# Kernel tuning notes

Measured on AMD Instinct MI355X. Metric: run time of the kernel, lower is better.

Reference implementation:

```python
import jax, jax.numpy as jnp
import numpy as np

NBITS = 4
GROUP = 128
K = 4096   # in_features
N = 4096   # out_features
M = 4096   # flattened batch*seq tokens
EPS = 32 // NBITS  # elements per packed int32 = 8
MASK = (1 << NBITS) - 1  # unpack_mask = 15


def setup_inputs() -> dict:
    key = jax.random.key(0)
    k1, k2, k3, k4, k5 = jax.random.split(key, 5)
    x = jax.random.normal(k1, (M, K), dtype=jnp.float32)
    # raw 4-bit quantized weights, layout [K, N] (i.e. W_q.t() from the torch module)
    nib = jax.random.randint(k2, (K, N), 0, 1 << NBITS, dtype=jnp.int32)
    # pack EPS nibbles per int32 along K, matching pack(): element j gets shift j*NBITS
    nib = nib.reshape(K // EPS, EPS, N)
    shifts = (jnp.arange(EPS, dtype=jnp.int32) * NBITS)[None, :, None]
    parts = nib << shifts  # disjoint bit ranges
    W_q_packed = parts[:, 0]
    for j in range(1, EPS):
        W_q_packed = W_q_packed | parts[:, j]
    W_q_packed = W_q_packed.astype(jnp.int32)  # [K//EPS, N]
    # group-wise scales/zeros: [K//GROUP, N] (scales.view(N,-1).t() layout)
    scales = (jax.random.uniform(k3, (K // GROUP, N), dtype=jnp.float32) + 0.5) * 0.01
    zeros = jax.random.uniform(k4, (K // GROUP, N), dtype=jnp.float32) * MASK
    bias = jax.random.normal(k5, (N,), dtype=jnp.float32) * 0.1
    return {"x": x, "W_q_packed": W_q_packed, "scales": scales, "zeros": zeros, "bias": bias}


def reference(x, W_q_packed, scales, zeros, bias):
    # unpack: w[k, n] = (packed[k//EPS, n] >> ((k % EPS) * NBITS)) & MASK
    shifts = (jnp.arange(EPS, dtype=jnp.int32) * NBITS)[None, :, None]
    w = (W_q_packed[:, None, :] >> shifts) & MASK  # [K//EPS, EPS, N]
    w = w.reshape(K, N).astype(jnp.float32)
    # group-wise asymmetric dequant (W_group_mode == 3): W = (w - z) * s
    s = jnp.repeat(scales, GROUP, axis=0)  # [K, N]
    z = jnp.repeat(zeros, GROUP, axis=0)   # [K, N]
    W = (w - z) * s
    out = x @ W + bias  # [M, N]
    return out
```

## Files before the change

### kernel.cpp

```cpp
#include <hip/hip_runtime.h>
#include <stdint.h>


#define M_DIM 4096
#define N_DIM 4096
#define K_DIM 4096

typedef __attribute__((ext_vector_type(8))) short short8;
typedef __attribute__((ext_vector_type(4))) float f32x4;

__device__ __forceinline__ unsigned short f2bf(float f) {
  uint32_t u = __builtin_bit_cast(uint32_t, f);
  u += 0x7fffu + ((u >> 16) & 1u);
  return (unsigned short)(u >> 16);
}

__global__ __launch_bounds__(256) void cvt_kernel(const float* __restrict__ x,
                                                  unsigned short* __restrict__ xb) {
  const int tid = threadIdx.x;
  const int total = (M_DIM * K_DIM) / 8;
  const float4* x4 = (const float4*)x;
  uint4* o8 = (uint4*)xb;
#pragma unroll
  for (int p = 0; p < 4; ++p) {
    int i = (p * 2048 + blockIdx.x) * 256 + tid;
    if (i < total) {
      float4 a = x4[2 * i], b = x4[2 * i + 1];
      uint4 o;
      o.x = (uint32_t)f2bf(a.x) | ((uint32_t)f2bf(a.y) << 16);
      o.y = (uint32_t)f2bf(a.z) | ((uint32_t)f2bf(a.w) << 16);
      o.z = (uint32_t)f2bf(b.x) | ((uint32_t)f2bf(b.y) << 16);
      o.w = (uint32_t)f2bf(b.z) | ((uint32_t)f2bf(b.w) << 16);
      o8[i] = o;
    }
  }
}

__global__ __launch_bounds__(256) void dequant_kernel(const int* __restrict__ Wq,
                                                      const float* __restrict__ scales,
                                                      const float* __restrict__ zeros,
                                                      unsigned short* __restrict__ wt) {
  __shared__ uint4 Ts[32 * 64];
  const int tid = threadIdx.x;
  const int blk = blockIdx.x;
  const int n0 = (blk & 127) * 32;
  const int gk0 = (blk >> 7) * 64;

#pragma unroll
  for (int p = 0; p < 8; ++p) {
    int e = p * 256 + tid;
    int n_l = e & 31;
    int gk_l = e >> 5;
    int gk = gk0 + gk_l;
    int n = n0 + n_l;
    int g = gk >> 4;
    uint32_t q = (uint32_t)Wq[gk * N_DIM + n];
    float s = scales[g * N_DIM + n];
    float z = zeros[g * N_DIM + n];
    unsigned short b[8];
#pragma unroll
    for (int j = 0; j < 8; ++j) {
      float f = ((float)((q >> (4 * j)) & 15u) - z) * s;
      b[j] = f2bf(f);
    }
    uint4 cell;
    cell.x = (uint32_t)b[0] | ((uint32_t)b[1] << 16);
    cell.y = (uint32_t)b[2] | ((uint32_t)b[3] << 16);
    cell.z = (uint32_t)b[4] | ((uint32_t)b[5] << 16);
    cell.w = (uint32_t)b[6] | ((uint32_t)b[7] << 16);
    Ts[n_l * 64 + (gk_l ^ (n_l & 7))] = cell;
  }
  __syncthreads();
  uint4* dst = (uint4*)wt;
#pragma unroll
  for (int p = 0; p < 8; ++p) {
    int n_l = p * 4 + (tid >> 6);
    int gk_l = tid & 63;
    uint4 cell = Ts[n_l * 64 + (gk_l ^ (n_l & 7))];
    dst[(size_t)(n0 + n_l) * (K_DIM / 8) + (gk0 + gk_l)] = cell;
  }
}


#define ASBUF(T) (As + ((T) & 1) * 1024)
#define BSBUF(T) (Bs + ((T) & 1) * 512)

#define GLDS(DST, SRC)                                                          \
  __builtin_amdgcn_global_load_lds(                                             \
      (const __attribute__((address_space(1))) void*)(SRC),                     \
      (__attribute__((address_space(3))) void*)(DST), 16, 0, 0)

#define STAGE(T)                                                                \
  {                                                                             \
    const unsigned short* as = Asrc + (size_t)(T) * 32;                         \
    const unsigned short* bs = Bsrc + (size_t)(T) * 32;                         \
    GLDS(ASBUF(T) + tid, as);                                                   \
    GLDS(ASBUF(T) + tid + 512, as + (size_t)128 * K_DIM);                       \
    GLDS(BSBUF(T) + tid, bs);                                                   \
  }

#define SB0 __builtin_amdgcn_sched_barrier(0)

__global__ __launch_bounds__(512, 4) void gemm_bt_kernel(
    const unsigned short* __restrict__ A, const unsigned short* __restrict__ Bt,
    const float* __restrict__ bias, float* __restrict__ C) {
  __shared__ short8 As[2 * 1024];
  __shared__ short8 Bs[2 * 512];

  const int tid = threadIdx.x;
  const int lane = tid & 63;
  const int w = tid >> 6;
  const int wm = w >> 1;
  const int wn = w & 1;

  const int b = blockIdx.x;
  const int xcd = b & 7;
  const int loc = b >> 3;
  const int nt = xcd * 4 + (loc & 3);
  const int mt = loc >> 2;
  const int m0 = mt * 256;
  const int n0 = nt * 128;

  const int srow = tid >> 2;
  const int skc = (tid & 3) ^ ((srow >> 1) & 3);
  const unsigned short* Asrc = A + (size_t)(m0 + srow) * K_DIM + skc * 8;
  const unsigned short* Bsrc = Bt + (size_t)(n0 + srow) * K_DIM + skc * 8;

  const int fr = lane & 15;
  const int fc = lane >> 4;
  const int kxs = fc ^ ((fr >> 1) & 3);
  const int a_b = (wm * 64 + fr) * 4 + kxs;
  const int b_b = (wn * 64 + fr) * 4 + kxs;

  f32x4 acc[4][4] = {};

  STAGE(0);
  asm volatile("s_waitcnt vmcnt(0)" ::: "memory");
  SB0;
  __builtin_amdgcn_s_barrier();

  for (int t = 0; t < 128; ++t) {
    if (t < 127) STAGE(t + 1);

    const short8* ASb = ASBUF(t);
    const short8* BSb = BSBUF(t);
    short8 af[4], bv[4];
#pragma unroll
    for (int mi = 0; mi < 4; ++mi) af[mi] = ASb[a_b + mi * 64];
#pragma unroll
    for (int ni = 0; ni < 4; ++ni) bv[ni] = BSb[b_b + ni * 64];

    __builtin_amdgcn_s_setprio(1);
#pragma unroll
    for (int mi = 0; mi < 4; ++mi)
#pragma unroll
      for (int ni = 0; ni < 4; ++ni)
        acc[mi][ni] = __builtin_amdgcn_mfma_f32_16x16x32_bf16(af[mi], bv[ni],
                                                              acc[mi][ni], 0, 0, 0);
    __builtin_amdgcn_s_setprio(0);

    if (t < 127) {
      asm volatile("s_waitcnt vmcnt(0)" ::: "memory");
      SB0;
      __builtin_amdgcn_s_barrier();
      SB0;
    }
  }

  const int rr = (lane >> 4) * 4;
#pragma unroll
  for (int ni = 0; ni < 4; ++ni) {
    const int gn = n0 + wn * 64 + ni * 16 + fr;
    const float bvv = bias[gn];
#pragma unroll
    for (int mi = 0; mi < 4; ++mi) {
      const int gm = m0 + wm * 64 + mi * 16 + rr;
#pragma unroll
      for (int r = 0; r < 4; ++r)
        C[(size_t)(gm + r) * N_DIM + gn] = acc[mi][ni][r] + bvv;
    }
  }
}

extern "C" void kernel_launch(void* const* d_in, const int* in_sizes, int n_in,
                              void* d_out, int out_size, void* d_ws, size_t ws_size,
                              hipStream_t stream) {
  const float* x = (const float*)d_in[0];
  const int* wq = (const int*)d_in[1];
  const float* sc = (const float*)d_in[2];
  const float* zr = (const float*)d_in[3];
  const float* bias = (const float*)d_in[4];
  float* out = (float*)d_out;

  unsigned short* xb = (unsigned short*)d_ws;
  unsigned short* wt = (unsigned short*)((char*)d_ws + (size_t)M_DIM * K_DIM * 2);

  cvt_kernel<<<dim3(2048), dim3(256), 0, stream>>>(x, xb);
  dequant_kernel<<<dim3(1024), dim3(256), 0, stream>>>(wq, sc, zr, wt);
  gemm_bt_kernel<<<dim3(512), dim3(512), 0, stream>>>(xb, wt, bias, out);
}
```

Measured before the change: 269.4 us.

## Pre-swizzle dequantized weights into MFMA fragment layout and load B directly to registers

```diff
diff --git a/kernel.cpp b/kernel.cpp
--- a/kernel.cpp
+++ b/kernel.cpp
@@ -39,133 +39,136 @@
 __global__ __launch_bounds__(256) void dequant_kernel(const int* __restrict__ Wq,
                                                       const float* __restrict__ scales,
                                                       const float* __restrict__ zeros,
-                                                      unsigned short* __restrict__ wt) {
-  __shared__ uint4 Ts[32 * 64];
+                                                      uint4* __restrict__ wf) {
   const int tid = threadIdx.x;
-  const int blk = blockIdx.x;
-  const int n0 = (blk & 127) * 32;
-  const int gk0 = (blk >> 7) * 64;
-
-#pragma unroll
-  for (int p = 0; p < 8; ++p) {
-    int e = p * 256 + tid;
-    int n_l = e & 31;
-    int gk_l = e >> 5;
-    int gk = gk0 + gk_l;
-    int n = n0 + n_l;
+#pragma unroll
+  for (int p = 0; p < 4; ++p) {
+    int c = (p * 2048 + blockIdx.x) * 256 + tid;
+    int lane = c & 63;
+    int F = c >> 6;
+    int t = F & 127;
+    int nf = F >> 7;
+    int fr = lane & 15, fc = lane >> 4;
+    int n = nf * 16 + fr;
+    int gk = t * 4 + fc;
     int g = gk >> 4;
     uint32_t q = (uint32_t)Wq[gk * N_DIM + n];
     float s = scales[g * N_DIM + n];
     float z = zeros[g * N_DIM + n];
-    unsigned short b[8];
+    unsigned short bb[8];
 #pragma unroll
     for (int j = 0; j < 8; ++j) {
       float f = ((float)((q >> (4 * j)) & 15u) - z) * s;
-      b[j] = f2bf(f);
+      bb[j] = f2bf(f);
     }
     uint4 cell;
-    cell.x = (uint32_t)b[0] | ((uint32_t)b[1] << 16);
-    cell.y = (uint32_t)b[2] | ((uint32_t)b[3] << 16);
-    cell.z = (uint32_t)b[4] | ((uint32_t)b[5] << 16);
-    cell.w = (uint32_t)b[6] | ((uint32_t)b[7] << 16);
-    Ts[n_l * 64 + (gk_l ^ (n_l & 7))] = cell;
-  }
-  __syncthreads();
-  uint4* dst = (uint4*)wt;
-#pragma unroll
-  for (int p = 0; p < 8; ++p) {
-    int n_l = p * 4 + (tid >> 6);
-    int gk_l = tid & 63;
-    uint4 cell = Ts[n_l * 64 + (gk_l ^ (n_l & 7))];
-    dst[(size_t)(n0 + n_l) * (K_DIM / 8) + (gk0 + gk_l)] = cell;
-  }
-}
-
-
-#define ASBUF(T) (As + ((T) & 1) * 1024)
-#define BSBUF(T) (Bs + ((T) & 1) * 512)
+    cell.x = (uint32_t)bb[0] | ((uint32_t)bb[1] << 16);
+    cell.y = (uint32_t)bb[2] | ((uint32_t)bb[3] << 16);
+    cell.z = (uint32_t)bb[4] | ((uint32_t)bb[5] << 16);
+    cell.w = (uint32_t)bb[6] | ((uint32_t)bb[7] << 16);
+    wf[c] = cell;
+  }
+}
+
 
 #define GLDS(DST, SRC)                                                          \
   __builtin_amdgcn_global_load_lds(                                             \
       (const __attribute__((address_space(1))) void*)(SRC),                     \
       (__attribute__((address_space(3))) void*)(DST), 16, 0, 0)
 
-#define STAGE(T)                                                                \
+#define SB0 __builtin_amdgcn_sched_barrier(0)
+#define VM2 asm volatile("s_waitcnt vmcnt(2)" ::: "memory")
+#define VM0 asm volatile("s_waitcnt vmcnt(0)" ::: "memory")
+
+#define LOADB(DST, T)                                                           \
   {                                                                             \
-    const unsigned short* as = Asrc + (size_t)(T) * 32;                         \
-    const unsigned short* bs = Bsrc + (size_t)(T) * 32;                         \
-    GLDS(ASBUF(T) + tid, as);                                                   \
-    GLDS(ASBUF(T) + tid + 512, as + (size_t)128 * K_DIM);                       \
-    GLDS(BSBUF(T) + tid, bs);                                                   \
-  }
-
-#define SB0 __builtin_amdgcn_sched_barrier(0)
-
-__global__ __launch_bounds__(512, 4) void gemm_bt_kernel(
-    const unsigned short* __restrict__ A, const unsigned short* __restrict__ Bt,
+    _Pragma("unroll") for (int ni = 0; ni < 4; ++ni)                            \
+        DST[ni] = __builtin_bit_cast(short8, Bf0[((size_t)ni * 128 + (T)) * 64]); \
+  }
+
+#define TILE(ACUR, AFAR, T, BVC, BVN, DO_LB, DO_SA, VMW)                        \
+  {                                                                             \
+    VMW;                                                                        \
+    SB0;                                                                        \
+    __builtin_amdgcn_s_barrier();                                               \
+    SB0;                                                                        \
+    if (DO_LB) LOADB(BVN, (T) + 1);                                             \
+    if (DO_SA) {                                                                \
+      const unsigned short* as_ = Asrc + (size_t)((T) + 2) * 32;                \
+      GLDS((AFAR) + tid, as_);                                                  \
+      GLDS((AFAR) + tid + 512, as_ + (size_t)128 * K_DIM);                      \
+    }                                                                           \
+    _Pragma("unroll") for (int mi = 0; mi < 4; ++mi) af[mi] = (ACUR)[a_b + mi * 64]; \
+    __builtin_amdgcn_s_setprio(1);                                              \
+    _Pragma("unroll") for (int mi = 0; mi < 4; ++mi)                            \
+        _Pragma("unroll") for (int ni = 0; ni < 4; ++ni)                        \
+            acc[mi][ni] = __builtin_amdgcn_mfma_f32_16x16x32_bf16(              \
+                af[mi], BVC[ni], acc[mi][ni], 0, 0, 0);                         \
+    __builtin_amdgcn_s_setprio(0);                                              \
+    _Pragma("unroll") for (int mi = 0; mi < 4; ++mi) af[mi] = (ACUR)[a_b + (mi + 4) * 64]; \
+    __builtin_amdgcn_s_setprio(1);                                              \
+    _Pragma("unroll") for (int mi = 0; mi < 4; ++mi)                            \
+        _Pragma("unroll") for (int ni = 0; ni < 4; ++ni)                        \
+            acc[mi + 4][ni] = __builtin_amdgcn_mfma_f32_16x16x32_bf16(          \
+                af[mi], BVC[ni], acc[mi + 4][ni], 0, 0, 0);                     \
+    __builtin_amdgcn_s_setprio(0);                                              \
+  }
+
+#define ROT3 { short8* tmp_ = a0; a0 = a1; a1 = a2; a2 = tmp_; }
+
+__global__ __launch_bounds__(512, 2) void gemm_bt_kernel(
+    const unsigned short* __restrict__ A, const uint4* __restrict__ Wf,
     const float* __restrict__ bias, float* __restrict__ C) {
-  __shared__ short8 As[2 * 1024];
-  __shared__ short8 Bs[2 * 512];
+  __shared__ short8 As[3 * 1024];
 
   const int tid = threadIdx.x;
   const int lane = tid & 63;
   const int w = tid >> 6;
-  const int wm = w >> 1;
-  const int wn = w & 1;
+  const int wm = w >> 2;
+  const int wn = w & 3;
 
   const int b = blockIdx.x;
   const int xcd = b & 7;
   const int loc = b >> 3;
-  const int nt = xcd * 4 + (loc & 3);
-  const int mt = loc >> 2;
+  const int nt = xcd * 2 + (loc & 1);
+  const int mt = loc >> 1;
   const int m0 = mt * 256;
-  const int n0 = nt * 128;
+  const int n0 = nt * 256;
 
   const int srow = tid >> 2;
   const int skc = (tid & 3) ^ ((srow >> 1) & 3);
   const unsigned short* Asrc = A + (size_t)(m0 + srow) * K_DIM + skc * 8;
-  const unsigned short* Bsrc = Bt + (size_t)(n0 + srow) * K_DIM + skc * 8;
+
+  const uint4* Bf0 = Wf + ((size_t)(n0 / 16 + wn * 4) * 128) * 64 + lane;
 
   const int fr = lane & 15;
   const int fc = lane >> 4;
   const int kxs = fc ^ ((fr >> 1) & 3);
-  const int a_b = (wm * 64 + fr) * 4 + kxs;
-  const int b_b = (wn * 64 + fr) * 4 + kxs;
-
-  f32x4 acc[4][4] = {};
-
-  STAGE(0);
-  asm volatile("s_waitcnt vmcnt(0)" ::: "memory");
-  SB0;
-  __builtin_amdgcn_s_barrier();
-
-  for (int t = 0; t < 128; ++t) {
-    if (t < 127) STAGE(t + 1);
-
-    const short8* ASb = ASBUF(t);
-    const short8* BSb = BSBUF(t);
-    short8 af[4], bv[4];
-#pragma unroll
-    for (int mi = 0; mi < 4; ++mi) af[mi] = ASb[a_b + mi * 64];
-#pragma unroll
-    for (int ni = 0; ni < 4; ++ni) bv[ni] = BSb[b_b + ni * 64];
-
-    __builtin_amdgcn_s_setprio(1);
-#pragma unroll
-    for (int mi = 0; mi < 4; ++mi)
-#pragma unroll
-      for (int ni = 0; ni < 4; ++ni)
-        acc[mi][ni] = __builtin_amdgcn_mfma_f32_16x16x32_bf16(af[mi], bv[ni],
-                                                              acc[mi][ni], 0, 0, 0);
-    __builtin_amdgcn_s_setprio(0);
-
-    if (t < 127) {
-      asm volatile("s_waitcnt vmcnt(0)" ::: "memory");
-      SB0;
-      __builtin_amdgcn_s_barrier();
-      SB0;
-    }
-  }
+  const int a_b = (wm * 128 + fr) * 4 + kxs;
+
+  f32x4 acc[8][4] = {};
+  short8 af[4];
+  short8 bvP[4], bvQ[4];
+
+  short8* a0 = As;
+  short8* a1 = As + 1024;
+  short8* a2 = As + 2048;
+
+  GLDS(a0 + tid, Asrc);
+  GLDS(a0 + tid + 512, Asrc + (size_t)128 * K_DIM);
+  LOADB(bvP, 0);
+  GLDS(a1 + tid, Asrc + 32);
+  GLDS(a1 + tid + 512, Asrc + 32 + (size_t)128 * K_DIM);
+
+  for (int t = 0; t < 126; t += 2) {
+    TILE(a0, a2, t, bvP, bvQ, 1, 1, VM2);
+    ROT3;
+    TILE(a0, a2, t + 1, bvQ, bvP, 1, 1, VM2);
+    ROT3;
+  }
+  TILE(a0, a2, 126, bvP, bvQ, 1, 0, VM2);
+  ROT3;
+  TILE(a0, a2, 127, bvQ, bvP, 0, 0, VM0);
 
   const int rr = (lane >> 4) * 4;
 #pragma unroll
@@ -173,8 +176,8 @@
     const int gn = n0 + wn * 64 + ni * 16 + fr;
     const float bvv = bias[gn];
 #pragma unroll
-    for (int mi = 0; mi < 4; ++mi) {
-      const int gm = m0 + wm * 64 + mi * 16 + rr;
+    for (int mi = 0; mi < 8; ++mi) {
+      const int gm = m0 + wm * 128 + mi * 16 + rr;
 #pragma unroll
       for (int r = 0; r < 4; ++r)
         C[(size_t)(gm + r) * N_DIM + gn] = acc[mi][ni][r] + bvv;
@@ -193,9 +196,9 @@
   float* out = (float*)d_out;
 
   unsigned short* xb = (unsigned short*)d_ws;
-  unsigned short* wt = (unsigned short*)((char*)d_ws + (size_t)M_DIM * K_DIM * 2);
+  uint4* wf = (uint4*)((char*)d_ws + (size_t)M_DIM * K_DIM * 2);
 
   cvt_kernel<<<dim3(2048), dim3(256), 0, stream>>>(x, xb);
-  dequant_kernel<<<dim3(1024), dim3(256), 0, stream>>>(wq, sc, zr, wt);
-  gemm_bt_kernel<<<dim3(512), dim3(512), 0, stream>>>(xb, wt, bias, out);
-}
+  dequant_kernel<<<dim3(2048), dim3(256), 0, stream>>>(wq, sc, zr, wf);
+  gemm_bt_kernel<<<dim3(256), dim3(512), 0, stream>>>(xb, wf, bias, out);
+}
```

New measurement: 276.4 us. +2.6%, slower.
